# Kernel optimization log

Measured on AMD Instinct MI355X. Metric: run time of the kernel, lower is better.

## Reference

```python
import jax, jax.numpy as jnp
import numpy as np


def setup_inputs() -> dict:
    key = jax.random.key(0)
    B, S, I, H, O = 32, 2048, 128, 512, 128
    ks = jax.random.split(key, 24)
    sc = 0.05
    d = {
        "x": jax.random.normal(ks[0], (B, S, I), jnp.float32),
        "h0": jnp.zeros((B, 2, H), jnp.float32),
        "l0_wxz": jax.random.normal(ks[1], (H, I)) * sc,
        "l0_bxz": jax.random.normal(ks[2], (H,)) * sc,
        "l0_whz": jax.random.normal(ks[3], (H, H)) * sc,
        "l0_wxr": jax.random.normal(ks[4], (H, I)) * sc,
        "l0_bxr": jax.random.normal(ks[5], (H,)) * sc,
        "l0_whr": jax.random.normal(ks[6], (H, H)) * sc,
        "l0_wxg": jax.random.normal(ks[7], (H, I)) * sc,
        "l0_bxg": jax.random.normal(ks[8], (H,)) * sc,
        "l0_whg": jax.random.normal(ks[9], (H, H)) * sc,
        "l1_wxz": jax.random.normal(ks[10], (H, H)) * sc,
        "l1_bxz": jax.random.normal(ks[11], (H,)) * sc,
        "l1_whz": jax.random.normal(ks[12], (H, H)) * sc,
        "l1_wxr": jax.random.normal(ks[13], (H, H)) * sc,
        "l1_bxr": jax.random.normal(ks[14], (H,)) * sc,
        "l1_whr": jax.random.normal(ks[15], (H, H)) * sc,
        "l1_wxg": jax.random.normal(ks[16], (H, H)) * sc,
        "l1_bxg": jax.random.normal(ks[17], (H,)) * sc,
        "l1_whg": jax.random.normal(ks[18], (H, H)) * sc,
        "wy": jax.random.normal(ks[19], (O, H)) * sc,
        "by": jax.random.normal(ks[20], (O,)) * sc,
    }
    return d


def _gru_cell(xt, h, wxz, bxz, whz, wxr, bxr, whr, wxg, bxg, whg):
    # z = sigmoid(Wxz x + bxz + Whz h); r = sigmoid(...); g = tanh(Wxg x + bxg + Whg (r*h))
    z = jax.nn.sigmoid(xt @ wxz.T + bxz + h @ whz.T)
    r = jax.nn.sigmoid(xt @ wxr.T + bxr + h @ whr.T)
    g = jnp.tanh(xt @ wxg.T + bxg + (r * h) @ whg.T)
    return z * h + (1.0 - z) * g


def reference(x, h0,
              l0_wxz, l0_bxz, l0_whz, l0_wxr, l0_bxr, l0_whr, l0_wxg, l0_bxg, l0_whg,
              l1_wxz, l1_bxz, l1_whz, l1_wxr, l1_bxr, l1_whr, l1_wxg, l1_bxg, l1_whg,
              wy, by):
    p0 = (l0_wxz, l0_bxz, l0_whz, l0_wxr, l0_bxr, l0_whr, l0_wxg, l0_bxg, l0_whg)
    p1 = (l1_wxz, l1_bxz, l1_whz, l1_wxr, l1_bxr, l1_whr, l1_wxg, l1_bxg, l1_whg)

    def step(carry, xt):  # xt: (B, I)
        h0_, h1_ = carry
        h0n = _gru_cell(xt, h0_, *p0)
        h1n = _gru_cell(h0n, h1_, *p1)
        y = h1n @ wy.T + by
        return (h0n, h1n), y

    xs = jnp.swapaxes(x, 0, 1)  # (S, B, I)
    init = (h0[:, 0, :], h0[:, 1, :])
    (hf0, hf1), ys = jax.lax.scan(step, init, xs)
    layer_output = jnp.swapaxes(ys, 0, 1)  # (B, S, O)
    hidden_state = jnp.stack([hf0, hf1], axis=1)  # (B, L, H)
    return layer_output, hidden_state
```

## Files before the change

### kernel.cpp

```cpp
#include <hip/hip_runtime.h>

typedef __bf16 bf16x8 __attribute__((ext_vector_type(8)));
typedef float f32x4 __attribute__((ext_vector_type(4)));
typedef unsigned short u16;
typedef unsigned int u32;
typedef unsigned long long u64;

#define MFMA16(a, b, c) __builtin_amdgcn_mfma_f32_16x16x32_bf16((a), (b), (c), 0, 0, 0)

namespace {
constexpr int kB = 32, kS = 2048, kI = 128, kH = 512, kO = 128;
constexpr int NC = 2;
constexpr int BPC = 16;
constexpr int L0WG = 16;
constexpr int WGC = 48;
constexpr int NSLOT = 4;
constexpr int NT = 2 * kS + 3;
constexpr long LOUT = (long)kB * kS * kO;
constexpr u32 POISON = 0xFFFFFFFFu;

constexpr size_t WS_FLG  = 0;
constexpr size_t WS_PUB0 = 8192;
constexpr size_t BUFSZ   = (size_t)NC * NSLOT * BPC * kH * 2;
constexpr size_t WS_PUB1 = WS_PUB0 + BUFSZ;
constexpr size_t WS_PR0  = WS_PUB1 + BUFSZ;
constexpr size_t WS_PR1  = WS_PR0 + BUFSZ;
constexpr size_t WS_WTS  = WS_PR1 + BUFSZ;

constexpr int W0H = 0;
constexpr int W0X = 786432;
constexpr int W1X = 983040;
constexpr int W1H = 1769472;
constexpr int WYO = 2555904;

constexpr int CSLOT = BPC * kH;
constexpr int CBUF  = NSLOT * CSLOT;
}

__device__ __forceinline__ u16 f2bf(float f) {
  u32 x = __float_as_uint(f);
  return (u16)((x + 0x7fffu + ((x >> 16) & 1u)) >> 16);
}

__device__ __forceinline__ u64 ld64a(const u64* p) {
  return __hip_atomic_load((u64*)p, __ATOMIC_RELAXED, __HIP_MEMORY_SCOPE_AGENT);
}
__device__ __forceinline__ u32 ld32a(const u32* p) {
  return __hip_atomic_load((u32*)p, __ATOMIC_RELAXED, __HIP_MEMORY_SCOPE_AGENT);
}
__device__ __forceinline__ bool bad(u64 v) {
  return ((u32)v == POISON) | ((u32)(v >> 32) == POISON);
}

struct Frags {
  u64 v[16];
  const u64* p;
  __device__ __forceinline__ void issue(const u16* base) {
    p = (const u64*)base;
#pragma unroll
    for (int s = 0; s < 8; ++s) {
      v[2 * s]     = ld64a(p + s * 8);
      v[2 * s + 1] = ld64a(p + s * 8 + 1);
    }
  }
  __device__ __forceinline__ bf16x8 get(int s) {
    u64 a = v[2 * s], b = v[2 * s + 1];
    while (bad(a)) a = ld64a(p + s * 8);
    while (bad(b)) b = ld64a(p + s * 8 + 1);
    union { u64 d[2]; bf16x8 f; } u_;
    u_.d[0] = a; u_.d[1] = b;
    return u_.f;
  }
};

__device__ __forceinline__ bf16x8 pack8(float4 a, float4 b) {
  union { u16 s[8]; bf16x8 v; } u_;
  u_.s[0] = f2bf(a.x); u_.s[1] = f2bf(a.y); u_.s[2] = f2bf(a.z); u_.s[3] = f2bf(a.w);
  u_.s[4] = f2bf(b.x); u_.s[5] = f2bf(b.y); u_.s[6] = f2bf(b.z); u_.s[7] = f2bf(b.w);
  return u_.v;
}

__global__ void prep_kernel(const float* whz0, const float* whr0, const float* whg0,
                            const float* wxz0, const float* wxr0, const float* wxg0,
                            const float* wxz1, const float* wxr1, const float* wxg1,
                            const float* whz1, const float* whr1, const float* whg1,
                            const float* wy, const float* h0in, char* ws) {
  u16* wts = (u16*)(ws + WS_WTS);
  int gid = blockIdx.x * blockDim.x + threadIdx.x;
  int stride = gridDim.x * blockDim.x;
  for (int i = gid; i < 786432; i += stride) {
    int g = i >> 18, r = i & 262143;
    wts[W0H + i] = f2bf((g == 0 ? whz0 : g == 1 ? whr0 : whg0)[r]);
  }
  for (int i = gid; i < 196608; i += stride) {
    int g = i >> 16, r = i & 65535;
    wts[W0X + i] = f2bf((g == 0 ? wxz0 : g == 1 ? wxr0 : wxg0)[r]);
  }
  for (int i = gid; i < 786432; i += stride) {
    int g = i >> 18, r = i & 262143;
    wts[W1X + i] = f2bf((g == 0 ? wxz1 : g == 1 ? wxr1 : wxg1)[r]);
  }
  for (int i = gid; i < 786432; i += stride) {
    int g = i >> 18, r = i & 262143;
    wts[W1H + i] = f2bf((g == 0 ? whz1 : g == 1 ? whr1 : whg1)[r]);
  }
  for (int i = gid; i < 65536; i += stride) wts[WYO + i] = f2bf(wy[i]);

  u32* r0 = (u32*)(ws + WS_PR0);
  u32* r1 = (u32*)(ws + WS_PR1);
  u32* b0 = (u32*)(ws + WS_PUB0);
  u32* b1 = (u32*)(ws + WS_PUB1);
  constexpr int NW = (int)(BUFSZ / 4);
  for (int i = gid; i < NW; i += stride) { r0[i] = POISON; r1[i] = POISON; }
  for (int i = gid; i < NW; i += stride) {
    int s = (i >> 12) & 3;
    if (s != 3) { b0[i] = POISON; b1[i] = POISON; }
  }
  u16* p0 = (u16*)(ws + WS_PUB0);
  u16* p1 = (u16*)(ws + WS_PUB1);
  for (int i = gid; i < NC * BPC * kH; i += stride) {
    int c = i / (BPC * kH), rem = i - c * (BPC * kH);
    int b = rem / kH, k = rem - b * kH;
    int bg = c * BPC + b;
    p0[c * CBUF + 3 * CSLOT + rem] = f2bf(h0in[(size_t)bg * 2 * kH + k]);
    p1[c * CBUF + 3 * CSLOT + rem] = f2bf(h0in[(size_t)bg * 2 * kH + kH + k]);
  }
  if (gid < 2048) ((u32*)(ws + WS_FLG))[gid] = 0u;
}

__device__ __forceinline__ void st_tile(float* base, f32x4 c, int q, int li) {
#pragma unroll
  for (int r = 0; r < 4; ++r) base[(q * 4 + r) * 17 + li] = c[r];
}

__device__ __forceinline__ void pub2(u16* base, int off, float v0, float v1) {
  u32 pk = (u32)f2bf(v0) | ((u32)f2bf(v1) << 16);
  __hip_atomic_store((u32*)(base + off), pk, __ATOMIC_RELAXED, __HIP_MEMORY_SCOPE_AGENT);
}
__device__ __forceinline__ void poison2(u16* base, int off) {
  __hip_atomic_store((u32*)(base + off), POISON, __ATOMIC_RELAXED, __HIP_MEMORY_SCOPE_AGENT);
}

__device__ __forceinline__ float sigm(float x) { return 1.f / (1.f + __expf(-x)); }
__device__ __forceinline__ float tanh_f(float x) {
  float te = __expf(-2.f * fabsf(x));
  return __builtin_copysignf((1.f - te) / (1.f + te), x);
}

__global__ __launch_bounds__(256, 1)
void gru_kernel(const float* __restrict__ xg, const float* __restrict__ h0in,
                const float* __restrict__ bxz0, const float* __restrict__ bxr0,
                const float* __restrict__ bxg0, const float* __restrict__ bxz1,
                const float* __restrict__ bxr1, const float* __restrict__ bxg1,
                const float* __restrict__ byv, float* __restrict__ out, char* ws) {
  const int cl = blockIdx.x / WGC;
  const int wid = blockIdx.x - cl * WGC;
  const bool isL0 = wid < L0WG;
  const int w0 = wid, w1 = wid - L0WG;
  const int tid = threadIdx.x;
  const int lane = tid & 63, wv = tid >> 6;
  const int q = lane >> 4, li = lane & 15;
  const int kh = wv & 1;
  const int nt = wv >> 1;
  const bool xside = wv < 2;

  u16* pub0 = (u16*)(ws + WS_PUB0) + (size_t)cl * CBUF;
  u16* pub1 = (u16*)(ws + WS_PUB1) + (size_t)cl * CBUF;
  u16* pr0  = (u16*)(ws + WS_PR0)  + (size_t)cl * CBUF;
  u16* pr1  = (u16*)(ws + WS_PR1)  + (size_t)cl * CBUF;
  const u16* wts = (const u16*)(ws + WS_WTS);
  u32* flags = (u32*)(ws + WS_FLG) + (size_t)cl * 1024;

  __shared__ __align__(16) float smem[5984];
  float* spA = smem;
  float* spB = smem;
  float* ypA = smem + 5440;

  bf16x8 wA[3][8];
  bf16x8 wE[8];
  if (isL0) {
    const int ci = w0 * 32 + nt * 16 + li;
#pragma unroll
    for (int g = 0; g < 3; ++g)
#pragma unroll
      for (int s = 0; s < 8; ++s)
        wA[g][s] = *(const bf16x8*)(wts + W0H + ((size_t)(g * kH + ci) * kH + kh * 256 + q * 8 + s * 32));
#pragma unroll
    for (int g = 0; g < 3; ++g)
#pragma unroll
      for (int s = 0; s < 2; ++s)
        wE[g * 2 + s] = *(const bf16x8*)(wts + W0X + ((size_t)(g * kH + ci) * kI + kh * 64 + q * 8 + s * 32));
  } else {
    const int ci = w1 * 16 + li;
    const int base = xside ? W1X : W1H;
#pragma unroll
    for (int g = 0; g < 3; ++g)
#pragma unroll
      for (int s = 0; s < 8; ++s)
        wA[g][s] = *(const bf16x8*)(wts + base + ((size_t)(g * kH + ci) * kH + kh * 256 + q * 8 + s * 32));
    if (!xside && w1 < 8) {
#pragma unroll
      for (int s = 0; s < 8; ++s)
        wE[s] = *(const bf16x8*)(wts + WYO + ((size_t)ci * kH + kh * 256 + q * 8 + s * 32));
    }
  }

  float2 bz2 = {0.f, 0.f}, br2 = {0.f, 0.f}, bg2 = {0.f, 0.f};
  float by_r = 0.f;
  float hm0r = 0.f, hm1r = 0.f;
  float zA0 = 0.f, zA1 = 0.f, gA0 = 0.f, gA1 = 0.f;
  if (isL0) {
    const int c0i = (tid & 15) * 2, bq = tid >> 4;
    bz2 = *(const float2*)(bxz0 + w0 * 32 + c0i);
    br2 = *(const float2*)(bxr0 + w0 * 32 + c0i);
    bg2 = *(const float2*)(bxg0 + w0 * 32 + c0i);
    const float* hp = h0in + (size_t)(cl * 16 + bq) * 2 * kH + w0 * 32 + c0i;
    hm0r = hp[0]; hm1r = hp[1];
  } else {
    const int c0i = (tid & 7) * 2, bq = tid >> 3;
    bz2 = *(const float2*)(bxz1 + w1 * 16 + c0i);
    br2 = *(const float2*)(bxr1 + w1 * 16 + c0i);
    bg2 = *(const float2*)(bxg1 + w1 * 16 + c0i);
    if (bq < 16) {
      const float* hp = h0in + (size_t)(cl * 16 + bq) * 2 * kH + kH + w1 * 16 + c0i;
      hm0r = hp[0]; hm1r = hp[1];
    }
    if (w1 < 8) by_r = byv[w1 * 16 + (tid & 15)];
  }

  for (int tk = 0; tk < NT; ++tk) {
    const bool ev = (tk & 1) == 0;
    const int t = tk >> 1;
    const int u = t - 1;
    const bool l0A = isL0 && ev && t < kS;
    const bool l0B = isL0 && !ev && t < kS;
    const bool l1A = !isL0 && ev && t >= 1 && t <= kS;
    const bool l1B = !isL0 && !ev && t >= 1 && t <= kS;
    const bool yAct = !isL0 && ev && w1 < 8 && t >= 2 && t <= kS + 1;

    u32 myfl = 0xFFFFFFFFu;
    if (lane < WGC) myfl = ld32a(flags + lane * 16);
    const u32 need = (tk >= 2) ? (u32)(tk - 2) : 0u;

    if (l0A) {
      Frags F;
      F.issue(pub0 + ((t + 3) & 3) * CSLOT + li * kH + kh * 256 + q * 8);
      const float* xr = xg + ((size_t)(cl * 16 + li) * kS + t) * kI + kh * 64 + q * 8;
      float4 xv0 = *(const float4*)xr;
      float4 xv1 = *(const float4*)(xr + 4);
      float4 xv2 = *(const float4*)(xr + 32);
      float4 xv3 = *(const float4*)(xr + 36);
      f32x4 hz = {0.f, 0.f, 0.f, 0.f}, hr = hz, xz = hz, xr2 = hz, xg2 = hz;
#pragma unroll
      for (int s = 0; s < 8; ++s) {
        bf16x8 a = F.get(s);
        hz = MFMA16(a, wA[0][s], hz);
        hr = MFMA16(a, wA[1][s], hr);
      }
      {
        bf16x8 a = pack8(xv0, xv1);
        xz  = MFMA16(a, wE[0], xz);
        xr2 = MFMA16(a, wE[2], xr2);
        xg2 = MFMA16(a, wE[4], xg2);
      }
      {
        bf16x8 a = pack8(xv2, xv3);
        xz  = MFMA16(a, wE[1], xz);
        xr2 = MFMA16(a, wE[3], xr2);
        xg2 = MFMA16(a, wE[5], xg2);
      }
      st_tile(spA + ((0 * 2 + nt) * 2 + kh) * 272, hz, q, li);
      st_tile(spA + ((1 * 2 + nt) * 2 + kh) * 272, hr, q, li);
      st_tile(spA + ((2 * 2 + nt) * 2 + kh) * 272, xz, q, li);
      st_tile(spA + ((3 * 2 + nt) * 2 + kh) * 272, xr2, q, li);
      st_tile(spA + ((4 * 2 + nt) * 2 + kh) * 272, xg2, q, li);
    } else if (!isL0 && ev) {
      if (xside) {
        if (l1A) {
          Frags F;
          F.issue(pub0 + (u & 3) * CSLOT + li * kH + kh * 256 + q * 8);
          f32x4 cz = {0.f, 0.f, 0.f, 0.f}, cr = cz, cg = cz;
#pragma unroll
          for (int s = 0; s < 8; ++s) {
            bf16x8 a = F.get(s);
            cz = MFMA16(a, wA[0][s], cz);
            cr = MFMA16(a, wA[1][s], cr);
            cg = MFMA16(a, wA[2][s], cg);
          }
          st_tile(spA + (2 * 2 + kh) * 272, cz, q, li);
          st_tile(spA + (3 * 2 + kh) * 272, cr, q, li);
          st_tile(spA + (4 * 2 + kh) * 272, cg, q, li);
        }
      } else {
        const bool rec = t >= 1 && t <= kS;
        const bool ym = (w1 < 8) && t >= 2 && t <= kS + 1;
        if (rec || ym) {
          Frags F;
          F.issue(pub1 + ((t + 2) & 3) * CSLOT + li * kH + kh * 256 + q * 8);
          f32x4 cz = {0.f, 0.f, 0.f, 0.f}, cr = cz, cy = cz;
#pragma unroll
          for (int s = 0; s < 8; ++s) {
            bf16x8 a = F.get(s);
            if (rec) {
              cz = MFMA16(a, wA[0][s], cz);
              cr = MFMA16(a, wA[1][s], cr);
            }
            if (ym) cy = MFMA16(a, wE[s], cy);
          }
          if (rec) {
            st_tile(spA + (0 * 2 + kh) * 272, cz, q, li);
            st_tile(spA + (1 * 2 + kh) * 272, cr, q, li);
          }
          if (ym) st_tile(ypA + kh * 272, cy, q, li);
        }
      }
    } else if (l0B) {
      Frags F;
      F.issue(pr0 + (t & 3) * CSLOT + li * kH + kh * 256 + q * 8);
      f32x4 cg = {0.f, 0.f, 0.f, 0.f};
#pragma unroll
      for (int s = 0; s < 8; ++s) cg = MFMA16(F.get(s), wA[2][s], cg);
      st_tile(spB + (nt * 2 + kh) * 272, cg, q, li);
    } else if (l1B && !xside) {
      Frags F;
      F.issue(pr1 + (u & 3) * CSLOT + li * kH + kh * 256 + q * 8);
      f32x4 cg = {0.f, 0.f, 0.f, 0.f};
#pragma unroll
      for (int s = 0; s < 8; ++s) cg = MFMA16(F.get(s), wA[2][s], cg);
      st_tile(spB + kh * 272, cg, q, li);
    }
    __syncthreads();

    while (__any((int)(myfl < need))) {
      if (lane < WGC) myfl = ld32a(flags + lane * 16);
    }

    if (l0A) {
      const int cp = tid & 15, b = tid >> 4;
      const int c0 = cp * 2, n2 = c0 >> 4, cc = c0 & 15, o = b * 17 + cc;
      float hz0 = spA[((0*2+n2)*2+0)*272 + o] + spA[((0*2+n2)*2+1)*272 + o];
      float hz1 = spA[((0*2+n2)*2+0)*272 + o+1] + spA[((0*2+n2)*2+1)*272 + o+1];
      float hr0 = spA[((1*2+n2)*2+0)*272 + o] + spA[((1*2+n2)*2+1)*272 + o];
      float hr1 = spA[((1*2+n2)*2+0)*272 + o+1] + spA[((1*2+n2)*2+1)*272 + o+1];
      float xz0 = spA[((2*2+n2)*2+0)*272 + o] + spA[((2*2+n2)*2+1)*272 + o];
      float xz1 = spA[((2*2+n2)*2+0)*272 + o+1] + spA[((2*2+n2)*2+1)*272 + o+1];
      float xr0 = spA[((3*2+n2)*2+0)*272 + o] + spA[((3*2+n2)*2+1)*272 + o];
      float xr1 = spA[((3*2+n2)*2+0)*272 + o+1] + spA[((3*2+n2)*2+1)*272 + o+1];
      float xg0 = spA[((4*2+n2)*2+0)*272 + o] + spA[((4*2+n2)*2+1)*272 + o];
      float xg1 = spA[((4*2+n2)*2+0)*272 + o+1] + spA[((4*2+n2)*2+1)*272 + o+1];
      zA0 = sigm(hz0 + xz0 + bz2.x);
      zA1 = sigm(hz1 + xz1 + bz2.y);
      float r0v = sigm(hr0 + xr0 + br2.x);
      float r1v = sigm(hr1 + xr1 + br2.y);
      gA0 = xg0 + bg2.x;
      gA1 = xg1 + bg2.y;
      const int off = b * kH + w0 * 32 + c0;
      pub2(pr0 + (t & 3) * CSLOT, off, r0v * hm0r, r1v * hm1r);
      poison2(pr0 + ((t + 2) & 3) * CSLOT, off);
    }
    if (l1A && tid < 128) {
      const int cp = tid & 7, b = tid >> 3;
      const int c0 = cp * 2, o = b * 17 + c0;
      float hz0 = spA[(0*2+0)*272 + o] + spA[(0*2+1)*272 + o];
      float hz1 = spA[(0*2+0)*272 + o+1] + spA[(0*2+1)*272 + o+1];
      float hr0 = spA[(1*2+0)*272 + o] + spA[(1*2+1)*272 + o];
      float hr1 = spA[(1*2+0)*272 + o+1] + spA[(1*2+1)*272 + o+1];
      float xz0 = spA[(2*2+0)*272 + o] + spA[(2*2+1)*272 + o];
      float xz1 = spA[(2*2+0)*272 + o+1] + spA[(2*2+1)*272 + o+1];
      float xr0 = spA[(3*2+0)*272 + o] + spA[(3*2+1)*272 + o];
      float xr1 = spA[(3*2+0)*272 + o+1] + spA[(3*2+1)*272 + o+1];
      float xg0 = spA[(4*2+0)*272 + o] + spA[(4*2+1)*272 + o];
      float xg1 = spA[(4*2+0)*272 + o+1] + spA[(4*2+1)*272 + o+1];
      zA0 = sigm(hz0 + xz0 + bz2.x);
      zA1 = sigm(hz1 + xz1 + bz2.y);
      float r0v = sigm(hr0 + xr0 + br2.x);
      float r1v = sigm(hr1 + xr1 + br2.y);
      gA0 = xg0 + bg2.x;
      gA1 = xg1 + bg2.y;
      const int off = b * kH + w1 * 16 + c0;
      pub2(pr1 + (u & 3) * CSLOT, off, r0v * hm0r, r1v * hm1r);
      poison2(pr1 + ((u + 2) & 3) * CSLOT, off);
    }
    if (yAct) {
      const int c = tid & 15, b = tid >> 4;
      float y = ypA[b * 17 + c] + ypA[272 + b * 17 + c] + by_r;
      out[((size_t)(cl * 16 + b) * kS + (t - 2)) * kO + w1 * 16 + c] = y;
    }
    if (l0B) {
      const int cp = tid & 15, b = tid >> 4;
      const int c0 = cp * 2, n2 = c0 >> 4, cc = c0 & 15, o = b * 17 + cc;
      float gh0 = spB[(n2*2+0)*272 + o] + spB[(n2*2+1)*272 + o];
      float gh1 = spB[(n2*2+0)*272 + o+1] + spB[(n2*2+1)*272 + o+1];
      float g0 = tanh_f(gA0 + gh0), g1 = tanh_f(gA1 + gh1);
      float hn0 = zA0 * hm0r + (1.f - zA0) * g0;
      float hn1 = zA1 * hm1r + (1.f - zA1) * g1;
      hm0r = hn0; hm1r = hn1;
      const int off = b * kH + w0 * 32 + c0;
      pub2(pub0 + (t & 3) * CSLOT, off, hn0, hn1);
      poison2(pub0 + ((t + 2) & 3) * CSLOT, off);
      if (t == kS - 1) {
        float* op = out + LOUT + (size_t)(cl * 16 + b) * 2 * kH + w0 * 32 + c0;
        op[0] = hn0; op[1] = hn1;
      }
    }
    if (l1B && tid < 128) {
      const int cp = tid & 7, b = tid >> 3;
      const int c0 = cp * 2, o = b * 17 + c0;
      float gh0 = spB[0 * 272 + o] + spB[1 * 272 + o];
      float gh1 = spB[0 * 272 + o+1] + spB[1 * 272 + o+1];
      float g0 = tanh_f(gA0 + gh0), g1 = tanh_f(gA1 + gh1);
      float hn0 = zA0 * hm0r + (1.f - zA0) * g0;
      float hn1 = zA1 * hm1r + (1.f - zA1) * g1;
      hm0r = hn0; hm1r = hn1;
      const int off = b * kH + w1 * 16 + c0;
      pub2(pub1 + (u & 3) * CSLOT, off, hn0, hn1);
      poison2(pub1 + ((u + 2) & 3) * CSLOT, off);
      if (u == kS - 1) {
        float* op = out + LOUT + (size_t)(cl * 16 + b) * 2 * kH + kH + w1 * 16 + c0;
        op[0] = hn0; op[1] = hn1;
      }
    }

    __syncthreads();
    if (tid == 0 && tk != NT - 1)
      __hip_atomic_store(flags + wid * 16, (u32)(tk + 1), __ATOMIC_RELAXED,
                         __HIP_MEMORY_SCOPE_AGENT);
  }
}

extern "C" void kernel_launch(void* const* d_in, const int* in_sizes, int n_in,
                              void* d_out, int out_size, void* d_ws, size_t ws_size,
                              hipStream_t stream) {
  (void)in_sizes; (void)n_in; (void)out_size; (void)ws_size;
  const float* x      = (const float*)d_in[0];
  const float* h0     = (const float*)d_in[1];
  const float* l0_wxz = (const float*)d_in[2];
  const float* l0_bxz = (const float*)d_in[3];
  const float* l0_whz = (const float*)d_in[4];
  const float* l0_wxr = (const float*)d_in[5];
  const float* l0_bxr = (const float*)d_in[6];
  const float* l0_whr = (const float*)d_in[7];
  const float* l0_wxg = (const float*)d_in[8];
  const float* l0_bxg = (const float*)d_in[9];
  const float* l0_whg = (const float*)d_in[10];
  const float* l1_wxz = (const float*)d_in[11];
  const float* l1_bxz = (const float*)d_in[12];
  const float* l1_whz = (const float*)d_in[13];
  const float* l1_wxr = (const float*)d_in[14];
  const float* l1_bxr = (const float*)d_in[15];
  const float* l1_whr = (const float*)d_in[16];
  const float* l1_wxg = (const float*)d_in[17];
  const float* l1_bxg = (const float*)d_in[18];
  const float* l1_whg = (const float*)d_in[19];
  const float* wy     = (const float*)d_in[20];
  const float* by     = (const float*)d_in[21];
  float* out = (float*)d_out;
  char* ws = (char*)d_ws;

  prep_kernel<<<512, 256, 0, stream>>>(l0_whz, l0_whr, l0_whg, l0_wxz, l0_wxr, l0_wxg,
                                       l1_wxz, l1_wxr, l1_wxg, l1_whz, l1_whr, l1_whg,
                                       wy, h0, ws);
  gru_kernel<<<NC * WGC, 256, 0, stream>>>(x, h0, l0_bxz, l0_bxr, l0_bxg,
                                           l1_bxz, l1_bxr, l1_bxg, by, out, ws);
}
```

Measured before the change: 16.51 ms.

## Restructure GRU persistent kernel to per-wavefront full-K tiles with wave-level flags

Each wavefront now owns a full 16-column output tile across the entire K=512 reduction instead of splitting K across wave pairs. This removes the LDS partial-sum reduction and most block-wide barriers. Synchronisation moves from per-workgroup flags with __syncthreads to per-wavefront flags that each wave checks just before publishing, and the workgroup count per cluster drops from 48 to 24. Gate math is done directly in MFMA accumulator registers, and publishing uses lane shuffles. The trade-off is roughly double the weight registers per wave and more flag polling traffic, with a risk of spilling or lower clocks.

Measured after the change: 31.41 ms. 1.9x slower.

```diff
diff --git a/kernel.cpp b/kernel.cpp
--- a/kernel.cpp
+++ b/kernel.cpp
@@ -12,15 +12,14 @@
 constexpr int kB = 32, kS = 2048, kI = 128, kH = 512, kO = 128;
 constexpr int NC = 2;
 constexpr int BPC = 16;
-constexpr int L0WG = 16;
-constexpr int WGC = 48;
 constexpr int NSLOT = 4;
-constexpr int NT = 2 * kS + 3;
+constexpr int NT = 2 * kS + 4;
 constexpr long LOUT = (long)kB * kS * kO;
 constexpr u32 POISON = 0xFFFFFFFFu;
+constexpr int BLKC = 24;
 
 constexpr size_t WS_FLG  = 0;
-constexpr size_t WS_PUB0 = 8192;
+constexpr size_t WS_PUB0 = 16384;
 constexpr size_t BUFSZ   = (size_t)NC * NSLOT * BPC * kH * 2;
 constexpr size_t WS_PUB1 = WS_PUB0 + BUFSZ;
 constexpr size_t WS_PR0  = WS_PUB1 + BUFSZ;
@@ -48,27 +47,37 @@
 __device__ __forceinline__ u32 ld32a(const u32* p) {
   return __hip_atomic_load((u32*)p, __ATOMIC_RELAXED, __HIP_MEMORY_SCOPE_AGENT);
 }
+__device__ __forceinline__ void st32a(u16* p, u32 v) {
+  __hip_atomic_store((u32*)p, v, __ATOMIC_RELAXED, __HIP_MEMORY_SCOPE_AGENT);
+}
 __device__ __forceinline__ bool bad(u64 v) {
   return ((u32)v == POISON) | ((u32)(v >> 32) == POISON);
 }
 
-struct Frags {
-  u64 v[16];
+struct Frag32 {
+  u64 v[32];
   const u64* p;
   __device__ __forceinline__ void issue(const u16* base) {
     p = (const u64*)base;
 #pragma unroll
-    for (int s = 0; s < 8; ++s) {
+    for (int s = 0; s < 16; ++s) {
       v[2 * s]     = ld64a(p + s * 8);
       v[2 * s + 1] = ld64a(p + s * 8 + 1);
     }
   }
-  __device__ __forceinline__ bf16x8 get(int s) {
-    u64 a = v[2 * s], b = v[2 * s + 1];
-    while (bad(a)) a = ld64a(p + s * 8);
-    while (bad(b)) b = ld64a(p + s * 8 + 1);
+  __device__ __forceinline__ void settle() {
+    while (true) {
+      bool any = false;
+#pragma unroll
+      for (int i = 0; i < 32; ++i) {
+        if (bad(v[i])) { any = true; v[i] = ld64a(p + (i >> 1) * 8 + (i & 1)); }
+      }
+      if (!any) break;
+    }
+  }
+  __device__ __forceinline__ bf16x8 frag(int s) const {
     union { u64 d[2]; bf16x8 f; } u_;
-    u_.d[0] = a; u_.d[1] = b;
+    u_.d[0] = v[2 * s]; u_.d[1] = v[2 * s + 1];
     return u_.f;
   }
 };
@@ -125,7 +134,7 @@
     p0[c * CBUF + 3 * CSLOT + rem] = f2bf(h0in[(size_t)bg * 2 * kH + k]);
     p1[c * CBUF + 3 * CSLOT + rem] = f2bf(h0in[(size_t)bg * 2 * kH + kH + k]);
   }
-  if (gid < 2048) ((u32*)(ws + WS_FLG))[gid] = 0u;
+  if (gid < NC * 2048) ((u32*)(ws + WS_FLG))[gid] = 0u;
 }
 
 __device__ __forceinline__ void st_tile(float* base, f32x4 c, int q, int li) {
@@ -133,12 +142,26 @@
   for (int r = 0; r < 4; ++r) base[(q * 4 + r) * 17 + li] = c[r];
 }
 
-__device__ __forceinline__ void pub2(u16* base, int off, float v0, float v1) {
-  u32 pk = (u32)f2bf(v0) | ((u32)f2bf(v1) << 16);
-  __hip_atomic_store((u32*)(base + off), pk, __ATOMIC_RELAXED, __HIP_MEMORY_SCOPE_AGENT);
-}
-__device__ __forceinline__ void poison2(u16* base, int off) {
-  __hip_atomic_store((u32*)(base + off), POISON, __ATOMIC_RELAXED, __HIP_MEMORY_SCOPE_AGENT);
+__device__ __forceinline__ void pub_tile(u16* slot, int C, int q, int li,
+                                         float v0, float v1, float v2, float v3) {
+  float o0 = __shfl_xor(v0, 1);
+  float o1 = __shfl_xor(v1, 1);
+  float o2 = __shfl_xor(v2, 1);
+  float o3 = __shfl_xor(v3, 1);
+  const int cp = C + (li & ~1);
+  if ((li & 1) == 0) {
+    st32a(slot + (q * 4 + 0) * kH + cp, (u32)f2bf(v0) | ((u32)f2bf(o0) << 16));
+    st32a(slot + (q * 4 + 1) * kH + cp, (u32)f2bf(v1) | ((u32)f2bf(o1) << 16));
+  } else {
+    st32a(slot + (q * 4 + 2) * kH + cp, (u32)f2bf(o2) | ((u32)f2bf(v2) << 16));
+    st32a(slot + (q * 4 + 3) * kH + cp, (u32)f2bf(o3) | ((u32)f2bf(v3) << 16));
+  }
+}
+
+__device__ __forceinline__ void poison_tile(u16* slot, int C, int lane) {
+  int row = lane >> 2;
+  __hip_atomic_store((u64*)(slot + row * kH + C) + (lane & 3),
+                     0xFFFFFFFFFFFFFFFFull, __ATOMIC_RELAXED, __HIP_MEMORY_SCOPE_AGENT);
 }
 
 __device__ __forceinline__ float sigm(float x) { return 1.f / (1.f + __expf(-x)); }
@@ -153,279 +176,248 @@
                 const float* __restrict__ bxg0, const float* __restrict__ bxz1,
                 const float* __restrict__ bxr1, const float* __restrict__ bxg1,
                 const float* __restrict__ byv, float* __restrict__ out, char* ws) {
-  const int cl = blockIdx.x / WGC;
-  const int wid = blockIdx.x - cl * WGC;
-  const bool isL0 = wid < L0WG;
-  const int w0 = wid, w1 = wid - L0WG;
+  const int cl = blockIdx.x / BLKC;
+  const int wid = blockIdx.x - cl * BLKC;
+  const bool isL0 = wid < 8;
   const int tid = threadIdx.x;
   const int lane = tid & 63, wv = tid >> 6;
   const int q = lane >> 4, li = lane & 15;
-  const int kh = wv & 1;
-  const int nt = wv >> 1;
-  const bool xside = wv < 2;
+  const int pairIdx = wv >> 1;
+  const bool xside = ((wv & 1) == 0);
+  const int myTile = isL0 ? (wid * 4 + wv) : ((wid - 8) * 2 + pairIdx);
+  const int wfid = isL0 ? myTile : (32 + myTile * 2 + (xside ? 0 : 1));
+  const int C = myTile * 16;
+  const int ci = C + li;
 
   u16* pub0 = (u16*)(ws + WS_PUB0) + (size_t)cl * CBUF;
   u16* pub1 = (u16*)(ws + WS_PUB1) + (size_t)cl * CBUF;
   u16* pr0  = (u16*)(ws + WS_PR0)  + (size_t)cl * CBUF;
   u16* pr1  = (u16*)(ws + WS_PR1)  + (size_t)cl * CBUF;
   const u16* wts = (const u16*)(ws + WS_WTS);
-  u32* flags = (u32*)(ws + WS_FLG) + (size_t)cl * 1024;
-
-  __shared__ __align__(16) float smem[5984];
-  float* spA = smem;
-  float* spB = smem;
-  float* ypA = smem + 5440;
-
-  bf16x8 wA[3][8];
-  bf16x8 wE[8];
+  u32* flags = (u32*)(ws + WS_FLG) + (size_t)cl * 2048;
+
+  __shared__ __align__(16) float lds[3264];
+
+  bf16x8 wM[3][16];
+  bf16x8 wX[3][4];
+  bf16x8 wY[16];
   if (isL0) {
-    const int ci = w0 * 32 + nt * 16 + li;
 #pragma unroll
     for (int g = 0; g < 3; ++g)
 #pragma unroll
-      for (int s = 0; s < 8; ++s)
-        wA[g][s] = *(const bf16x8*)(wts + W0H + ((size_t)(g * kH + ci) * kH + kh * 256 + q * 8 + s * 32));
+      for (int s = 0; s < 16; ++s)
+        wM[g][s] = *(const bf16x8*)(wts + W0H + ((size_t)(g * kH + ci) * kH + q * 8 + s * 32));
 #pragma unroll
     for (int g = 0; g < 3; ++g)
 #pragma unroll
-      for (int s = 0; s < 2; ++s)
-        wE[g * 2 + s] = *(const bf16x8*)(wts + W0X + ((size_t)(g * kH + ci) * kI + kh * 64 + q * 8 + s * 32));
+      for (int s = 0; s < 4; ++s)
+        wX[g][s] = *(const bf16x8*)(wts + W0X + ((size_t)(g * kH + ci) * kI + q * 8 + s * 32));
   } else {
-    const int ci = w1 * 16 + li;
     const int base = xside ? W1X : W1H;
 #pragma unroll
     for (int g = 0; g < 3; ++g)
 #pragma unroll
-      for (int s = 0; s < 8; ++s)
-        wA[g][s] = *(const bf16x8*)(wts + base + ((size_t)(g * kH + ci) * kH + kh * 256 + q * 8 + s * 32));
-    if (!xside && w1 < 8) {
-#pragma unroll
-      for (int s = 0; s < 8; ++s)
-        wE[s] = *(const bf16x8*)(wts + WYO + ((size_t)ci * kH + kh * 256 + q * 8 + s * 32));
+      for (int s = 0; s < 16; ++s)
+        wM[g][s] = *(const bf16x8*)(wts + base + ((size_t)(g * kH + ci) * kH + q * 8 + s * 32));
+    if (xside && myTile < 8) {
+#pragma unroll
+      for (int s = 0; s < 16; ++s)
+        wY[s] = *(const bf16x8*)(wts + WYO + ((size_t)ci * kH + q * 8 + s * 32));
     }
   }
 
-  float2 bz2 = {0.f, 0.f}, br2 = {0.f, 0.f}, bg2 = {0.f, 0.f};
-  float by_r = 0.f;
-  float hm0r = 0.f, hm1r = 0.f;
-  float zA0 = 0.f, zA1 = 0.f, gA0 = 0.f, gA1 = 0.f;
+  float bz = 0.f, br = 0.f, bg = 0.f, byr = 0.f;
+  float hm[4] = {0.f, 0.f, 0.f, 0.f};
+  float zS[4] = {0.f, 0.f, 0.f, 0.f};
+  float gS[4] = {0.f, 0.f, 0.f, 0.f};
   if (isL0) {
-    const int c0i = (tid & 15) * 2, bq = tid >> 4;
-    bz2 = *(const float2*)(bxz0 + w0 * 32 + c0i);
-    br2 = *(const float2*)(bxr0 + w0 * 32 + c0i);
-    bg2 = *(const float2*)(bxg0 + w0 * 32 + c0i);
-    const float* hp = h0in + (size_t)(cl * 16 + bq) * 2 * kH + w0 * 32 + c0i;
-    hm0r = hp[0]; hm1r = hp[1];
-  } else {
-    const int c0i = (tid & 7) * 2, bq = tid >> 3;
-    bz2 = *(const float2*)(bxz1 + w1 * 16 + c0i);
-    br2 = *(const float2*)(bxr1 + w1 * 16 + c0i);
-    bg2 = *(const float2*)(bxg1 + w1 * 16 + c0i);
-    if (bq < 16) {
-      const float* hp = h0in + (size_t)(cl * 16 + bq) * 2 * kH + kH + w1 * 16 + c0i;
-      hm0r = hp[0]; hm1r = hp[1];
-    }
-    if (w1 < 8) by_r = byv[w1 * 16 + (tid & 15)];
+    bz = bxz0[ci]; br = bxr0[ci]; bg = bxg0[ci];
+#pragma unroll
+    for (int i = 0; i < 4; ++i)
+      hm[i] = h0in[(size_t)(cl * 16 + q * 4 + i) * 2 * kH + ci];
+  } else if (!xside) {
+    bz = bxz1[ci]; br = bxr1[ci]; bg = bxg1[ci];
+#pragma unroll
+    for (int i = 0; i < 4; ++i)
+      hm[i] = h0in[(size_t)(cl * 16 + q * 4 + i) * 2 * kH + kH + ci];
+  } else if (myTile < 8) {
+    byr = byv[ci];
   }
 
   for (int tk = 0; tk < NT; ++tk) {
     const bool ev = (tk & 1) == 0;
-    const int t = tk >> 1;
-    const int u = t - 1;
-    const bool l0A = isL0 && ev && t < kS;
-    const bool l0B = isL0 && !ev && t < kS;
-    const bool l1A = !isL0 && ev && t >= 1 && t <= kS;
-    const bool l1B = !isL0 && !ev && t >= 1 && t <= kS;
-    const bool yAct = !isL0 && ev && w1 < 8 && t >= 2 && t <= kS + 1;
-
-    u32 myfl = 0xFFFFFFFFu;
-    if (lane < WGC) myfl = ld32a(flags + lane * 16);
+    const int T = tk >> 1;
+    const int u = T - 1;
+
+    u32 fa = ld32a(flags + lane * 16);
+    u32 fb = ld32a(flags + (lane + 32) * 16);
     const u32 need = (tk >= 2) ? (u32)(tk - 2) : 0u;
-
-    if (l0A) {
-      Frags F;
-      F.issue(pub0 + ((t + 3) & 3) * CSLOT + li * kH + kh * 256 + q * 8);
-      const float* xr = xg + ((size_t)(cl * 16 + li) * kS + t) * kI + kh * 64 + q * 8;
-      float4 xv0 = *(const float4*)xr;
-      float4 xv1 = *(const float4*)(xr + 4);
-      float4 xv2 = *(const float4*)(xr + 32);
-      float4 xv3 = *(const float4*)(xr + 36);
-      f32x4 hz = {0.f, 0.f, 0.f, 0.f}, hr = hz, xz = hz, xr2 = hz, xg2 = hz;
-#pragma unroll
-      for (int s = 0; s < 8; ++s) {
-        bf16x8 a = F.get(s);
-        hz = MFMA16(a, wA[0][s], hz);
-        hr = MFMA16(a, wA[1][s], hr);
-      }
-      {
-        bf16x8 a = pack8(xv0, xv1);
-        xz  = MFMA16(a, wE[0], xz);
-        xr2 = MFMA16(a, wE[2], xr2);
-        xg2 = MFMA16(a, wE[4], xg2);
-      }
-      {
-        bf16x8 a = pack8(xv2, xv3);
-        xz  = MFMA16(a, wE[1], xz);
-        xr2 = MFMA16(a, wE[3], xr2);
-        xg2 = MFMA16(a, wE[5], xg2);
-      }
-      st_tile(spA + ((0 * 2 + nt) * 2 + kh) * 272, hz, q, li);
-      st_tile(spA + ((1 * 2 + nt) * 2 + kh) * 272, hr, q, li);
-      st_tile(spA + ((2 * 2 + nt) * 2 + kh) * 272, xz, q, li);
-      st_tile(spA + ((3 * 2 + nt) * 2 + kh) * 272, xr2, q, li);
-      st_tile(spA + ((4 * 2 + nt) * 2 + kh) * 272, xg2, q, li);
-    } else if (!isL0 && ev) {
-      if (xside) {
-        if (l1A) {
-          Frags F;
-          F.issue(pub0 + (u & 3) * CSLOT + li * kH + kh * 256 + q * 8);
-          f32x4 cz = {0.f, 0.f, 0.f, 0.f}, cr = cz, cg = cz;
-#pragma unroll
-          for (int s = 0; s < 8; ++s) {
-            bf16x8 a = F.get(s);
-            cz = MFMA16(a, wA[0][s], cz);
-            cr = MFMA16(a, wA[1][s], cr);
-            cg = MFMA16(a, wA[2][s], cg);
-          }
-          st_tile(spA + (2 * 2 + kh) * 272, cz, q, li);
-          st_tile(spA + (3 * 2 + kh) * 272, cr, q, li);
-          st_tile(spA + (4 * 2 + kh) * 272, cg, q, li);
+#define GATE_ENFORCE()                                        \
+    while (__any((int)((fa < need) | (fb < need)))) {         \
+      fa = ld32a(flags + lane * 16);                          \
+      fb = ld32a(flags + (lane + 32) * 16);                   \
+    }
+
+    if (isL0) {
+      if (ev) {
+        if (T < kS) {
+          Frag32 F;
+          F.issue(pub0 + ((T + 3) & 3) * CSLOT + li * kH + q * 8);
+          const float* xr = xg + ((size_t)(cl * 16 + li) * kS + T) * kI + q * 8;
+          float4 a0 = *(const float4*)(xr);
+          float4 a1 = *(const float4*)(xr + 4);
+          float4 a2 = *(const float4*)(xr + 32);
+          float4 a3 = *(const float4*)(xr + 36);
+          float4 a4 = *(const float4*)(xr + 64);
+          float4 a5 = *(const float4*)(xr + 68);
+          float4 a6 = *(const float4*)(xr + 96);
+          float4 a7 = *(const float4*)(xr + 100);
+          bf16x8 xf0 = pack8(a0, a1), xf1 = pack8(a2, a3);
+          bf16x8 xf2 = pack8(a4, a5), xf3 = pack8(a6, a7);
+          F.settle();
+          f32x4 hz = {0.f, 0.f, 0.f, 0.f}, hr = hz, xz = hz, xr2 = hz, xg2 = hz;
+#pragma unroll
+          for (int s = 0; s < 16; ++s) {
+            bf16x8 a = F.frag(s);
+            hz = MFMA16(a, wM[0][s], hz);
+            hr = MFMA16(a, wM[1][s], hr);
+          }
+          xz  = MFMA16(xf0, wX[0][0], xz);  xz  = MFMA16(xf1, wX[0][1], xz);
+          xz  = MFMA16(xf2, wX[0][2], xz);  xz  = MFMA16(xf3, wX[0][3], xz);
+          xr2 = MFMA16(xf0, wX[1][0], xr2); xr2 = MFMA16(xf1, wX[1][1], xr2);
+          xr2 = MFMA16(xf2, wX[1][2], xr2); xr2 = MFMA16(xf3, wX[1][3], xr2);
+          xg2 = MFMA16(xf0, wX[2][0], xg2); xg2 = MFMA16(xf1, wX[2][1], xg2);
+          xg2 = MFMA16(xf2, wX[2][2], xg2); xg2 = MFMA16(xf3, wX[2][3], xg2);
+          float rh[4];
+#pragma unroll
+          for (int i = 0; i < 4; ++i) {
+            float z = sigm(hz[i] + xz[i] + bz);
+            float r = sigm(hr[i] + xr2[i] + br);
+            zS[i] = z; gS[i] = xg2[i] + bg;
+            rh[i] = r * hm[i];
+          }
+          GATE_ENFORCE();
+          pub_tile(pr0 + (T & 3) * CSLOT, C, q, li, rh[0], rh[1], rh[2], rh[3]);
+          poison_tile(pr0 + ((T + 2) & 3) * CSLOT, C, lane);
         }
       } else {
-        const bool rec = t >= 1 && t <= kS;
-        const bool ym = (w1 < 8) && t >= 2 && t <= kS + 1;
-        if (rec || ym) {
-          Frags F;
-          F.issue(pub1 + ((t + 2) & 3) * CSLOT + li * kH + kh * 256 + q * 8);
-          f32x4 cz = {0.f, 0.f, 0.f, 0.f}, cr = cz, cy = cz;
-#pragma unroll
-          for (int s = 0; s < 8; ++s) {
-            bf16x8 a = F.get(s);
-            if (rec) {
-              cz = MFMA16(a, wA[0][s], cz);
-              cr = MFMA16(a, wA[1][s], cr);
-            }
-            if (ym) cy = MFMA16(a, wE[s], cy);
-          }
-          if (rec) {
-            st_tile(spA + (0 * 2 + kh) * 272, cz, q, li);
-            st_tile(spA + (1 * 2 + kh) * 272, cr, q, li);
-          }
-          if (ym) st_tile(ypA + kh * 272, cy, q, li);
+        if (T < kS) {
+          Frag32 F;
+          F.issue(pr0 + (T & 3) * CSLOT + li * kH + q * 8);
+          F.settle();
+          f32x4 cg = {0.f, 0.f, 0.f, 0.f};
+#pragma unroll
+          for (int s = 0; s < 16; ++s) cg = MFMA16(F.frag(s), wM[2][s], cg);
+#pragma unroll
+          for (int i = 0; i < 4; ++i) {
+            float g = tanh_f(gS[i] + cg[i]);
+            hm[i] = zS[i] * hm[i] + (1.f - zS[i]) * g;
+          }
+          GATE_ENFORCE();
+          pub_tile(pub0 + (T & 3) * CSLOT, C, q, li, hm[0], hm[1], hm[2], hm[3]);
+          poison_tile(pub0 + ((T + 2) & 3) * CSLOT, C, lane);
+          if (T == kS - 1) {
+#pragma unroll
+            for (int i = 0; i < 4; ++i)
+              out[LOUT + (size_t)(cl * 16 + q * 4 + i) * 2 * kH + ci] = hm[i];
+          }
         }
       }
-    } else if (l0B) {
-      Frags F;
-      F.issue(pr0 + (t & 3) * CSLOT + li * kH + kh * 256 + q * 8);
-      f32x4 cg = {0.f, 0.f, 0.f, 0.f};
-#pragma unroll
-      for (int s = 0; s < 8; ++s) cg = MFMA16(F.get(s), wA[2][s], cg);
-      st_tile(spB + (nt * 2 + kh) * 272, cg, q, li);
-    } else if (l1B && !xside) {
-      Frags F;
-      F.issue(pr1 + (u & 3) * CSLOT + li * kH + kh * 256 + q * 8);
-      f32x4 cg = {0.f, 0.f, 0.f, 0.f};
-#pragma unroll
-      for (int s = 0; s < 8; ++s) cg = MFMA16(F.get(s), wA[2][s], cg);
-      st_tile(spB + kh * 272, cg, q, li);
-    }
-    __syncthreads();
-
-    while (__any((int)(myfl < need))) {
-      if (lane < WGC) myfl = ld32a(flags + lane * 16);
-    }
-
-    if (l0A) {
-      const int cp = tid & 15, b = tid >> 4;
-      const int c0 = cp * 2, n2 = c0 >> 4, cc = c0 & 15, o = b * 17 + cc;
-      float hz0 = spA[((0*2+n2)*2+0)*272 + o] + spA[((0*2+n2)*2+1)*272 + o];
-      float hz1 = spA[((0*2+n2)*2+0)*272 + o+1] + spA[((0*2+n2)*2+1)*272 + o+1];
-      float hr0 = spA[((1*2+n2)*2+0)*272 + o] + spA[((1*2+n2)*2+1)*272 + o];
-      float hr1 = spA[((1*2+n2)*2+0)*272 + o+1] + spA[((1*2+n2)*2+1)*272 + o+1];
-      float xz0 = spA[((2*2+n2)*2+0)*272 + o] + spA[((2*2+n2)*2+1)*272 + o];
-      float xz1 = spA[((2*2+n2)*2+0)*272 + o+1] + spA[((2*2+n2)*2+1)*272 + o+1];
-      float xr0 = spA[((3*2+n2)*2+0)*272 + o] + spA[((3*2+n2)*2+1)*272 + o];
-      float xr1 = spA[((3*2+n2)*2+0)*272 + o+1] + spA[((3*2+n2)*2+1)*272 + o+1];
-      float xg0 = spA[((4*2+n2)*2+0)*272 + o] + spA[((4*2+n2)*2+1)*272 + o];
-      float xg1 = spA[((4*2+n2)*2+0)*272 + o+1] + spA[((4*2+n2)*2+1)*272 + o+1];
-      zA0 = sigm(hz0 + xz0 + bz2.x);
-      zA1 = sigm(hz1 + xz1 + bz2.y);
-      float r0v = sigm(hr0 + xr0 + br2.x);
-      float r1v = sigm(hr1 + xr1 + br2.y);
-      gA0 = xg0 + bg2.x;
-      gA1 = xg1 + bg2.y;
-      const int off = b * kH + w0 * 32 + c0;
-      pub2(pr0 + (t & 3) * CSLOT, off, r0v * hm0r, r1v * hm1r);
-      poison2(pr0 + ((t + 2) & 3) * CSLOT, off);
-    }
-    if (l1A && tid < 128) {
-      const int cp = tid & 7, b = tid >> 3;
-      const int c0 = cp * 2, o = b * 17 + c0;
-      float hz0 = spA[(0*2+0)*272 + o] + spA[(0*2+1)*272 + o];
-      float hz1 = spA[(0*2+0)*272 + o+1] + spA[(0*2+1)*272 + o+1];
-      float hr0 = spA[(1*2+0)*272 + o] + spA[(1*2+1)*272 + o];
-      float hr1 = spA[(1*2+0)*272 + o+1] + spA[(1*2+1)*272 + o+1];
-      float xz0 = spA[(2*2+0)*272 + o] + spA[(2*2+1)*272 + o];
-      float xz1 = spA[(2*2+0)*272 + o+1] + spA[(2*2+1)*272 + o+1];
-      float xr0 = spA[(3*2+0)*272 + o] + spA[(3*2+1)*272 + o];
-      float xr1 = spA[(3*2+0)*272 + o+1] + spA[(3*2+1)*272 + o+1];
-      float xg0 = spA[(4*2+0)*272 + o] + spA[(4*2+1)*272 + o];
-      float xg1 = spA[(4*2+0)*272 + o+1] + spA[(4*2+1)*272 + o+1];
-      zA0 = sigm(hz0 + xz0 + bz2.x);
-      zA1 = sigm(hz1 + xz1 + bz2.y);
-      float r0v = sigm(hr0 + xr0 + br2.x);
-      float r1v = sigm(hr1 + xr1 + br2.y);
-      gA0 = xg0 + bg2.x;
-      gA1 = xg1 + bg2.y;
-      const int off = b * kH + w1 * 16 + c0;
-      pub2(pr1 + (u & 3) * CSLOT, off, r0v * hm0r, r1v * hm1r);
-      poison2(pr1 + ((u + 2) & 3) * CSLOT, off);
-    }
-    if (yAct) {
-      const int c = tid & 15, b = tid >> 4;
-      float y = ypA[b * 17 + c] + ypA[272 + b * 17 + c] + by_r;
-      out[((size_t)(cl * 16 + b) * kS + (t - 2)) * kO + w1 * 16 + c] = y;
-    }
-    if (l0B) {
-      const int cp = tid & 15, b = tid >> 4;
-      const int c0 = cp * 2, n2 = c0 >> 4, cc = c0 & 15, o = b * 17 + cc;
-      float gh0 = spB[(n2*2+0)*272 + o] + spB[(n2*2+1)*272 + o];
-      float gh1 = spB[(n2*2+0)*272 + o+1] + spB[(n2*2+1)*272 + o+1];
-      float g0 = tanh_f(gA0 + gh0), g1 = tanh_f(gA1 + gh1);
-      float hn0 = zA0 * hm0r + (1.f - zA0) * g0;
-      float hn1 = zA1 * hm1r + (1.f - zA1) * g1;
-      hm0r = hn0; hm1r = hn1;
-      const int off = b * kH + w0 * 32 + c0;
-      pub2(pub0 + (t & 3) * CSLOT, off, hn0, hn1);
-      poison2(pub0 + ((t + 2) & 3) * CSLOT, off);
-      if (t == kS - 1) {
-        float* op = out + LOUT + (size_t)(cl * 16 + b) * 2 * kH + w0 * 32 + c0;
-        op[0] = hn0; op[1] = hn1;
+    } else {
+      if (ev) {
+        const bool act = (u >= 0) && (u < kS);
+        f32x4 czh = {0.f, 0.f, 0.f, 0.f}, crh = czh;
+        if (xside) {
+          if (act) {
+            Frag32 F;
+            F.issue(pub0 + (u & 3) * CSLOT + li * kH + q * 8);
+            F.settle();
+            f32x4 cz = {0.f, 0.f, 0.f, 0.f}, cr = cz, cg = cz;
+#pragma unroll
+            for (int s = 0; s < 16; ++s) {
+              bf16x8 a = F.frag(s);
+              cz = MFMA16(a, wM[0][s], cz);
+              cr = MFMA16(a, wM[1][s], cr);
+              cg = MFMA16(a, wM[2][s], cg);
+            }
+            float* tb = lds + ((pairIdx * 2 + (T & 1)) * 3) * 272;
+            st_tile(tb, cz, q, li);
+            st_tile(tb + 272, cr, q, li);
+            st_tile(tb + 544, cg, q, li);
+          }
+        } else {
+          if (act) {
+            Frag32 F;
+            F.issue(pub1 + ((u + 3) & 3) * CSLOT + li * kH + q * 8);
+            F.settle();
+#pragma unroll
+            for (int s = 0; s < 16; ++s) {
+              bf16x8 a = F.frag(s);
+              czh = MFMA16(a, wM[0][s], czh);
+              crh = MFMA16(a, wM[1][s], crh);
+            }
+          }
+        }
+        __syncthreads();
+        if (!xside && act) {
+          const float* tb = lds + ((pairIdx * 2 + (T & 1)) * 3) * 272;
+          float rh[4];
+#pragma unroll
+          for (int i = 0; i < 4; ++i) {
+            const int o = (q * 4 + i) * 17 + li;
+            float z = sigm(czh[i] + tb[o] + bz);
+            float r = sigm(crh[i] + tb[272 + o] + br);
+            zS[i] = z; gS[i] = tb[544 + o] + bg;
+            rh[i] = r * hm[i];
+          }
+          GATE_ENFORCE();
+          pub_tile(pr1 + (u & 3) * CSLOT, C, q, li, rh[0], rh[1], rh[2], rh[3]);
+          poison_tile(pr1 + ((u + 2) & 3) * CSLOT, C, lane);
+        }
+      } else {
+        if (!xside) {
+          if (u >= 0 && u < kS) {
+            Frag32 F;
+            F.issue(pr1 + (u & 3) * CSLOT + li * kH + q * 8);
+            F.settle();
+            f32x4 cg = {0.f, 0.f, 0.f, 0.f};
+#pragma unroll
+            for (int s = 0; s < 16; ++s) cg = MFMA16(F.frag(s), wM[2][s], cg);
+#pragma unroll
+            for (int i = 0; i < 4; ++i) {
+              float g = tanh_f(gS[i] + cg[i]);
+              hm[i] = zS[i] * hm[i] + (1.f - zS[i]) * g;
+            }
+            GATE_ENFORCE();
+            pub_tile(pub1 + (u & 3) * CSLOT, C, q, li, hm[0], hm[1], hm[2], hm[3]);
+            poison_tile(pub1 + ((u + 1) & 3) * CSLOT, C, lane);
+            if (u == kS - 1) {
+#pragma unroll
+              for (int i = 0; i < 4; ++i)
+                out[LOUT + (size_t)(cl * 16 + q * 4 + i) * 2 * kH + kH + ci] = hm[i];
+            }
+          }
+        } else if (myTile < 8) {
+          const int w = T - 2;
+          if (w >= 0 && w < kS) {
+            Frag32 F;
+            F.issue(pub1 + (w & 3) * CSLOT + li * kH + q * 8);
+            F.settle();
+            f32x4 cy = {0.f, 0.f, 0.f, 0.f};
+#pragma unroll
+            for (int s = 0; s < 16; ++s) cy = MFMA16(F.frag(s), wY[s], cy);
+#pragma unroll
+            for (int i = 0; i < 4; ++i)
+              out[((size_t)(cl * 16 + q * 4 + i) * kS + w) * kO + ci] = cy[i] + byr;
+          }
+        }
       }
     }
-    if (l1B && tid < 128) {
-      const int cp = tid & 7, b = tid >> 3;
-      const int c0 = cp * 2, o = b * 17 + c0;
-      float gh0 = spB[0 * 272 + o] + spB[1 * 272 + o];
-      float gh1 = spB[0 * 272 + o+1] + spB[1 * 272 + o+1];
-      float g0 = tanh_f(gA0 + gh0), g1 = tanh_f(gA1 + gh1);
-      float hn0 = zA0 * hm0r + (1.f - zA0) * g0;
-      float hn1 = zA1 * hm1r + (1.f - zA1) * g1;
-      hm0r = hn0; hm1r = hn1;
-      const int off = b * kH + w1 * 16 + c0;
-      pub2(pub1 + (u & 3) * CSLOT, off, hn0, hn1);
-      poison2(pub1 + ((u + 2) & 3) * CSLOT, off);
-      if (u == kS - 1) {
-        float* op = out + LOUT + (size_t)(cl * 16 + b) * 2 * kH + kH + w1 * 16 + c0;
-        op[0] = hn0; op[1] = hn1;
-      }
-    }
-
-    __syncthreads();
-    if (tid == 0 && tk != NT - 1)
-      __hip_atomic_store(flags + wid * 16, (u32)(tk + 1), __ATOMIC_RELAXED,
-                         __HIP_MEMORY_SCOPE_AGENT);
-  }
+
+    if (lane == 0 && tk != NT - 1)
+      st32a((u16*)(flags + wfid * 16), (u32)(tk + 1));
+  }
+#undef GATE_ENFORCE
 }
 
 extern "C" void kernel_launch(void* const* d_in, const int* in_sizes, int n_in,
@@ -460,6 +452,6 @@
   prep_kernel<<<512, 256, 0, stream>>>(l0_whz, l0_whr, l0_whg, l0_wxz, l0_wxr, l0_wxg,
                                        l1_wxz, l1_wxr, l1_wxg, l1_whz, l1_whr, l1_whg,
                                        wy, h0, ws);
-  gru_kernel<<<NC * WGC, 256, 0, stream>>>(x, h0, l0_bxz, l0_bxr, l0_bxg,
-                                           l1_bxz, l1_bxr, l1_bxg, by, out, ws);
-}
+  gru_kernel<<<NC * BLKC, 256, 0, stream>>>(x, h0, l0_bxz, l0_bxr, l0_bxg,
+                                            l1_bxz, l1_bxr, l1_bxg, by, out, ws);
+}
```
